# Optimization experiments

Measured on AMD Instinct MI355X. Metric: run time of the kernel, lower is better.

The kernel has to match this reference:

```python
import jax, jax.numpy as jnp
import numpy as np

N_NODES = 50000
N_EDGES = 500000


def setup_inputs() -> dict:
    key = jax.random.key(0)
    ks = jax.random.split(key, 24)
    p = {}
    p['x_feat'] = jax.random.normal(ks[0], (N_NODES, 24), dtype=jnp.float32)
    p['edge_index'] = jax.random.randint(ks[1], (2, N_EDGES), 0, N_NODES)
    p['edge_attr'] = jax.random.uniform(ks[2], (N_EDGES, 16), dtype=jnp.float32)
    def lin(k, fan_in, shape):
        b = 1.0 / np.sqrt(fan_in)
        return jax.random.uniform(k, shape, jnp.float32, -b, b)
    # group-0 input projection: 24 -> 32
    p['lin_prep_W'] = lin(ks[3], 24, (24, 32)); p['lin_prep_b'] = lin(ks[4], 24, (32,))
    # prep tube: 32 -> 16
    p['tube_W'] = lin(ks[5], 32, (32, 16)); p['tube_b'] = lin(ks[6], 32, (16,))
    # shared edge-attr trunk: 16 -> 32 -> 16
    p['edge_W1'] = lin(ks[7], 16, (16, 32)); p['edge_b1'] = lin(ks[8], 16, (32,))
    p['edge_W2'] = lin(ks[9], 32, (32, 16)); p['edge_b2'] = lin(ks[10], 32, (16,))
    # conv1: in=16, out=8 per aggr (mean, max, add)
    p['conv1_edge_W'] = lin(ks[11], 16, (3, 16, 16 * 8)); p['conv1_edge_b'] = lin(ks[12], 16, (3, 16 * 8))
    p['conv1_root_W'] = lin(ks[13], 16, (3, 16, 8)); p['conv1_bias'] = lin(ks[14], 16, (3, 8))
    # conv2: in=24, out=8 per aggr
    p['conv2_edge_W'] = lin(ks[15], 16, (3, 16, 24 * 8)); p['conv2_edge_b'] = lin(ks[16], 16, (3, 24 * 8))
    p['conv2_root_W'] = lin(ks[17], 24, (3, 24, 8)); p['conv2_bias'] = lin(ks[18], 24, (3, 8))
    # output head: 24 -> 2
    p['out_W'] = lin(ks[19], 24, (24, 2)); p['out_b'] = lin(ks[20], 24, (2,))
    return p


def _nnconv(x, e_repr, src, dst, edge_W, edge_b, root_W, bias, n_nodes):
    # x: [N, in]; e_repr: [E, 16]; edge_W: [3, 16, in*out]
    d_in = x.shape[1]
    x_src = x[src]  # [E, in]
    deg = jax.ops.segment_sum(jnp.ones_like(src, dtype=x.dtype), dst, num_segments=n_nodes)  # [N]
    outs = []
    for a, aggr in enumerate(('mean', 'max', 'add')):
        W_e = (e_repr @ edge_W[a] + edge_b[a]).reshape(e_repr.shape[0], d_in, -1)  # [E, in, out]
        msg = jnp.einsum('ei,eio->eo', x_src, W_e)  # [E, out]
        if aggr == 'add':
            agg = jax.ops.segment_sum(msg, dst, num_segments=n_nodes)
        elif aggr == 'mean':
            agg = jax.ops.segment_sum(msg, dst, num_segments=n_nodes) / jnp.maximum(deg, 1.0)[:, None]
        else:
            agg = jax.ops.segment_max(msg, dst, num_segments=n_nodes)
            agg = jnp.where(deg[:, None] > 0, agg, 0.0)  # no-neighbor nodes -> 0
        outs.append(agg + x @ root_W[a] + bias[a])
    return jax.nn.relu(jnp.concatenate(outs, axis=1))  # [N, 3*out]


def reference(x_feat, edge_index, edge_attr, lin_prep_W, lin_prep_b, tube_W, tube_b,
              edge_W1, edge_b1, edge_W2, edge_b2,
              conv1_edge_W, conv1_edge_b, conv1_root_W, conv1_bias,
              conv2_edge_W, conv2_edge_b, conv2_root_W, conv2_bias,
              out_W, out_b):
    n_nodes = x_feat.shape[0]
    src, dst = edge_index[0], edge_index[1]
    # node prep: group projection + tube (relu acts, dropout=0 -> identity)
    x = jax.nn.relu(x_feat @ lin_prep_W + lin_prep_b)       # [N, 32]
    x = jax.nn.relu(x @ tube_W + tube_b)                    # [N, 16]
    # shared edge-attr trunk (last activation = sigmoid), computed once
    e = jax.nn.relu(edge_attr @ edge_W1 + edge_b1)
    e_repr = jax.nn.sigmoid(e @ edge_W2 + edge_b2)          # [E, 16]
    # hop 1 and hop 2 of edge-conditioned NNConv with mean/max/add aggregators
    x = _nnconv(x, e_repr, src, dst, conv1_edge_W, conv1_edge_b, conv1_root_W, conv1_bias, n_nodes)  # [N, 24]
    x = _nnconv(x, e_repr, src, dst, conv2_edge_W, conv2_edge_b, conv2_root_W, conv2_bias, n_nodes)  # [N, 24]
    logits = x @ out_W + out_b                              # [N, 2]
    scores = jax.nn.softmax(logits, axis=1)
    return (logits, scores)
```

## Files before the change

### kernel.cpp

```cpp
#include <hip/hip_runtime.h>

#define BS 256

__device__ __forceinline__ unsigned short f2bf(float f) {
    unsigned x = __float_as_uint(f);
    return (unsigned short)((x + 0x7fffu + ((x >> 16) & 1u)) >> 16);
}
__device__ __forceinline__ unsigned pack2bf(float a, float b) {
    return (unsigned)f2bf(a) | ((unsigned)f2bf(b) << 16);
}
__device__ __forceinline__ void unpack2(unsigned u, float* d) {
    d[0] = __uint_as_float(u << 16);
    d[1] = __uint_as_float(u & 0xFFFF0000u);
}
__device__ __forceinline__ void unpack8(uint4 v, float* d) {
    unpack2(v.x, d); unpack2(v.y, d + 2); unpack2(v.z, d + 4); unpack2(v.w, d + 6);
}
__device__ __forceinline__ uint4 pack8bf(const float* r) {
    return make_uint4(pack2bf(r[0], r[1]), pack2bf(r[2], r[3]),
                      pack2bf(r[4], r[5]), pack2bf(r[6], r[7]));
}

__global__ __launch_bounds__(BS) void prep_deg_kernel(
    const float* __restrict__ xf,
    const float* __restrict__ W1, const float* __restrict__ b1,
    const float* __restrict__ W2, const float* __restrict__ b2,
    float* __restrict__ x16,
    const int* __restrict__ srcA, const int* __restrict__ dstA,
    int* __restrict__ cntS, int* __restrict__ cntD,
    int* __restrict__ jS, int* __restrict__ jD,
    int N, int E, int nbPrep)
{
    if ((int)blockIdx.x < nbPrep) {
        int n = blockIdx.x * BS + threadIdx.x;
        bool valid = n < N;
        int nn = valid ? n : 0;
        float a[24];
#pragma unroll
        for (int i = 0; i < 24; i += 4)
            *(float4*)(a + i) = *(const float4*)(xf + (size_t)nn * 24 + i);
        float h[32];
#pragma unroll
        for (int j = 0; j < 32; j++) {
            float s = b1[j];
#pragma unroll
            for (int i = 0; i < 24; i++) s = fmaf(a[i], W1[i * 32 + j], s);
            h[j] = fmaxf(s, 0.f);
        }
        if (!valid) return;
#pragma unroll
        for (int j = 0; j < 16; j++) {
            float s = b2[j];
#pragma unroll
            for (int i = 0; i < 32; i++) s = fmaf(h[i], W2[i * 16 + j], s);
            x16[(size_t)n * 16 + j] = fmaxf(s, 0.f);
        }
    } else {
        int tid = (blockIdx.x - nbPrep) * BS + threadIdx.x;
        if (tid < E) {
            jS[tid] = atomicAdd(&cntS[srcA[tid]], 1);
        } else if (tid < 2 * E) {
            int e = tid - E;
            jD[e] = atomicAdd(&cntD[dstA[e]], 1);
        }
    }
}

__global__ __launch_bounds__(BS) void offs_ynode16_kernel(
    const int* __restrict__ cntS, const int* __restrict__ cntD,
    int* __restrict__ offsS, int* __restrict__ offsD,
    int* __restrict__ cursS, int* __restrict__ cursD,
    const float* __restrict__ x,
    const float* __restrict__ W,
    const float* __restrict__ B,
    const float* __restrict__ RW,
    const float* __restrict__ RB,
    unsigned short* __restrict__ Y,
    float* __restrict__ root,
    int N, int nbOff, int nbY3)
{
    if ((int)blockIdx.x < nbOff) {
        int n = blockIdx.x * BS + threadIdx.x;
        int lane = threadIdx.x & 63;
        bool valid = n < N;
        int dS = valid ? cntS[n] : 0;
        int dD = valid ? cntD[n] : 0;
        int sS = dS, sD = dD;
#pragma unroll
        for (int o = 1; o < 64; o <<= 1) {
            int tS = __shfl_up(sS, o);
            int tD = __shfl_up(sD, o);
            if (lane >= o) { sS += tS; sD += tD; }
        }
        int totS = __shfl(sS, 63);
        int totD = __shfl(sD, 63);
        int baseS = 0, baseD = 0;
        if (lane == 63) {
            baseS = atomicAdd(cursS, totS);
            baseD = atomicAdd(cursD, totD);
        }
        baseS = __shfl(baseS, 63);
        baseD = __shfl(baseD, 63);
        if (valid) {
            offsS[n] = baseS + sS - dS;
            offsD[n] = baseD + sD - dD;
        }
    } else {
        const int IN = 16;
        __shared__ float w_lds[16 * 24];
        int t = threadIdx.x;
        int blk = blockIdx.x - nbOff;
        int kb = blk / nbY3;
        int xb = blk - kb * nbY3;

        for (int idx = t; idx < IN * 24; idx += BS) {
            int i = idx / 24;
            int j = idx - i * 24;
            int a = j >> 3, o = j & 7;
            float v;
            if (kb < 16)       v = W[(((size_t)a * 16 + kb) * IN + i) * 8 + o];
            else if (kb == 16) v = B[((size_t)a * IN + i) * 8 + o];
            else               v = RW[((size_t)a * IN + i) * 8 + o];
            w_lds[idx] = v;
        }
        __syncthreads();

        int tid = xb * BS + t;
        int n = tid / 3;
        int a = tid - n * 3;
        if (n >= N) return;

        float xv[IN];
#pragma unroll
        for (int i = 0; i < IN; i += 4)
            *(float4*)(xv + i) = *(const float4*)(x + (size_t)n * IN + i);

        float acc[8];
#pragma unroll
        for (int o = 0; o < 8; o++) acc[o] = 0.f;
        const float* wb = w_lds + a * 8;
#pragma unroll
        for (int i = 0; i < IN; i++) {
            float xi = xv[i];
#pragma unroll
            for (int o = 0; o < 8; o++)
                acc[o] = fmaf(xi, wb[i * 24 + o], acc[o]);
        }

        if (kb < 17) {
            *(uint4*)(Y + ((size_t)kb * N + n) * 24 + a * 8) = pack8bf(acc);
        } else {
            float* pr = root + (size_t)n * 24 + a * 8;
            *(float4*)(pr)     = make_float4(acc[0] + RB[a*8+0], acc[1] + RB[a*8+1],
                                             acc[2] + RB[a*8+2], acc[3] + RB[a*8+3]);
            *(float4*)(pr + 4) = make_float4(acc[4] + RB[a*8+4], acc[5] + RB[a*8+5],
                                             acc[6] + RB[a*8+6], acc[7] + RB[a*8+7]);
        }
    }
}

__global__ __launch_bounds__(BS) void er_fill_kernel(
    const int* __restrict__ srcA, const int* __restrict__ dstA,
    const int* __restrict__ jS, const int* __restrict__ jD,
    const int* __restrict__ offsS, const int* __restrict__ offsD,
    const float* __restrict__ eattr,
    const float* __restrict__ eW1, const float* __restrict__ eb1,
    const float* __restrict__ eW2, const float* __restrict__ eb2,
    uint4* __restrict__ erec, int E)
{
    int e = blockIdx.x * BS + threadIdx.x;
    if (e >= E) return;
    int s = srcA[e], d = dstA[e];
    int p = offsS[s] + jS[e];
    int q = offsD[d] + jD[e];

    float ea[16];
#pragma unroll
    for (int i = 0; i < 16; i += 4)
        *(float4*)(ea + i) = *(const float4*)(eattr + (size_t)e * 16 + i);
    float h[32];
#pragma unroll
    for (int j = 0; j < 32; j++) {
        float t = eb1[j];
#pragma unroll
        for (int i = 0; i < 16; i++) t = fmaf(ea[i], eW1[i * 32 + j], t);
        h[j] = fmaxf(t, 0.f);
    }
    float er[16];
#pragma unroll
    for (int j = 0; j < 16; j++) {
        float t = eb2[j];
#pragma unroll
        for (int i = 0; i < 32; i++) t = fmaf(h[i], eW2[i * 16 + j], t);
        er[j] = 1.f / (1.f + __expf(-t));
    }
    unsigned w[8];
#pragma unroll
    for (int j = 0; j < 8; j++) w[j] = pack2bf(er[2 * j], er[2 * j + 1]);
    uint4* rp = erec + (size_t)p * 4;
    rp[0] = make_uint4((unsigned)s, (unsigned)q, w[0], w[1]);
    rp[1] = make_uint4(w[2], w[3], w[4], w[5]);
    rp[2] = make_uint4(w[6], w[7], 0u, 0u);
    rp[3] = make_uint4(0u, 0u, 0u, 0u);
}

template <int IN>
__global__ __launch_bounds__(BS) void ynode_kernel(const float* __restrict__ x,
                                                   const float* __restrict__ W,
                                                   const float* __restrict__ B,
                                                   const float* __restrict__ RW,
                                                   const float* __restrict__ RB,
                                                   unsigned short* __restrict__ Y,
                                                   float* __restrict__ root, int N)
{
    __shared__ float w_lds[IN * 24];
    int t = threadIdx.x;
    int k = blockIdx.y;

    for (int idx = t; idx < IN * 24; idx += BS) {
        int i = idx / 24;
        int j = idx - i * 24;
        int a = j >> 3, o = j & 7;
        float v;
        if (k < 16)       v = W[(((size_t)a * 16 + k) * IN + i) * 8 + o];
        else if (k == 16) v = B[((size_t)a * IN + i) * 8 + o];
        else              v = RW[((size_t)a * IN + i) * 8 + o];
        w_lds[idx] = v;
    }
    __syncthreads();

    int tid = blockIdx.x * BS + t;
    int n = tid / 3;
    int a = tid - n * 3;
    if (n >= N) return;

    float xv[IN];
#pragma unroll
    for (int i = 0; i < IN; i += 4)
        *(float4*)(xv + i) = *(const float4*)(x + (size_t)n * IN + i);

    float acc[8];
#pragma unroll
    for (int o = 0; o < 8; o++) acc[o] = 0.f;
    const float* wb = w_lds + a * 8;
#pragma unroll
    for (int i = 0; i < IN; i++) {
        float xi = xv[i];
#pragma unroll
        for (int o = 0; o < 8; o++)
            acc[o] = fmaf(xi, wb[i * 24 + o], acc[o]);
    }

    if (k < 17) {
        *(uint4*)(Y + ((size_t)k * N + n) * 24 + a * 8) = pack8bf(acc);
    } else {
        float* pr = root + (size_t)n * 24 + a * 8;
        *(float4*)(pr)     = make_float4(acc[0] + RB[a*8+0], acc[1] + RB[a*8+1],
                                         acc[2] + RB[a*8+2], acc[3] + RB[a*8+3]);
        *(float4*)(pr + 4) = make_float4(acc[4] + RB[a*8+4], acc[5] + RB[a*8+5],
                                         acc[6] + RB[a*8+6], acc[7] + RB[a*8+7]);
    }
}

__global__ __launch_bounds__(BS) void msg_kernel(
    const uint4* __restrict__ erec,
    const unsigned short* __restrict__ Y,
    unsigned short* __restrict__ msg16,
    int N, int E)
{
    int tid = blockIdx.x * BS + threadIdx.x;
    int p = tid / 3;
    int j = tid - p * 3;
    if (p >= E) return;

    const uint4* rp = erec + (size_t)p * 4;
    uint4 r0 = rp[0];
    uint4 r1 = rp[1];
    uint4 r2 = rp[2];
    unsigned s = r0.x, q = r0.y;

    float er[16];
    unpack2(r0.z, er); unpack2(r0.w, er + 2);
    unpack8(r1, er + 4);
    unpack2(r2.x, er + 12); unpack2(r2.y, er + 14);

    const unsigned short* yb = Y + (size_t)s * 24 + j * 8;
    size_t kstride = (size_t)N * 24;

    float acc[8];
    unpack8(*(const uint4*)(yb + 16 * kstride), acc);
#pragma unroll
    for (int k = 0; k < 16; k++) {
        float t[8];
        unpack8(*(const uint4*)(yb + (size_t)k * kstride), t);
        float ek = er[k];
#pragma unroll
        for (int o = 0; o < 8; o++) acc[o] = fmaf(ek, t[o], acc[o]);
    }
    unsigned short* mrow = msg16 + (size_t)q * 32;
    *(uint4*)(mrow + j * 8) = pack8bf(acc);
    if (j == 0) *(uint4*)(mrow + 24) = make_uint4(0, 0, 0, 0);
}

template <bool FUSE_HEAD>
__global__ __launch_bounds__(BS) void gather_kernel(
    const unsigned short* __restrict__ msg16,
    const int* __restrict__ offs,
    const int* __restrict__ degi,
    const float* __restrict__ root,
    float* __restrict__ out,
    const float* __restrict__ oW, const float* __restrict__ ob,
    int N)
{
    int n = (blockIdx.x * BS + threadIdx.x) >> 6;
    if (n >= N) return;
    int lane = threadIdx.x & 63;
    int c = lane & 3;
    int r = lane >> 2;

    int off = offs[n];
    int d = degi[n];

    float s[8], m[8];
#pragma unroll
    for (int o = 0; o < 8; o++) { s[o] = 0.f; m[o] = -3.402823466e38f; }

    if (c < 3) {
        const unsigned short* base = msg16 + (size_t)off * 32 + c * 8;
        for (int j = r; j < d; j += 16) {
            uint4 v = *(const uint4*)(base + (size_t)j * 32);
            float t[8];
            unpack8(v, t);
#pragma unroll
            for (int o = 0; o < 8; o++) {
                s[o] += t[o];
                m[o] = fmaxf(m[o], t[o]);
            }
        }
    }
#pragma unroll
    for (int mask = 4; mask < 64; mask <<= 1) {
#pragma unroll
        for (int o = 0; o < 8; o++) {
            s[o] += __shfl_xor(s[o], mask);
            m[o] = fmaxf(m[o], __shfl_xor(m[o], mask));
        }
    }

    bool active = (lane < 3);
    float rr[8];
    if (active) {
        float inv = 1.f / fmaxf((float)d, 1.f);
        const float* pr = root + (size_t)n * 24 + lane * 8;
        float4 r0 = *(const float4*)(pr);
        float4 r1 = *(const float4*)(pr + 4);
        float rb[8] = {r0.x, r0.y, r0.z, r0.w, r1.x, r1.y, r1.z, r1.w};
#pragma unroll
        for (int o = 0; o < 8; o++) {
            float agg = (lane == 0) ? s[o] * inv
                      : (lane == 1) ? ((d > 0) ? m[o] : 0.f)
                      : s[o];
            rr[o] = fmaxf(rb[o] + agg, 0.f);
        }
    }

    if (!FUSE_HEAD) {
        if (active) {
            float* po = out + (size_t)n * 24 + lane * 8;
            *(float4*)(po)     = make_float4(rr[0], rr[1], rr[2], rr[3]);
            *(float4*)(po + 4) = make_float4(rr[4], rr[5], rr[6], rr[7]);
        }
    } else {
        float l0p = 0.f, l1p = 0.f;
        if (active) {
#pragma unroll
            for (int o = 0; o < 8; o++) {
                l0p = fmaf(rr[o], oW[(lane * 8 + o) * 2 + 0], l0p);
                l1p = fmaf(rr[o], oW[(lane * 8 + o) * 2 + 1], l1p);
            }
        }
        float l0 = __shfl(l0p, 0) + __shfl(l0p, 1) + __shfl(l0p, 2);
        float l1 = __shfl(l1p, 0) + __shfl(l1p, 1) + __shfl(l1p, 2);
        if (lane == 0) {
            l0 += ob[0]; l1 += ob[1];
            out[2 * (size_t)n + 0] = l0;
            out[2 * (size_t)n + 1] = l1;
            float mx = fmaxf(l0, l1);
            float e0 = __expf(l0 - mx), e1 = __expf(l1 - mx);
            float sm = e0 + e1;
            out[2 * (size_t)N + 2 * (size_t)n + 0] = e0 / sm;
            out[2 * (size_t)N + 2 * (size_t)n + 1] = e1 / sm;
        }
    }
}

extern "C" void kernel_launch(void* const* d_in, const int* in_sizes, int n_in,
                              void* d_out, int out_size, void* d_ws, size_t ws_size,
                              hipStream_t stream)
{
    const float* x_feat = (const float*)d_in[0];
    const int*   eidx   = (const int*)d_in[1];
    const float* eattr  = (const float*)d_in[2];
    const float* lpW = (const float*)d_in[3];
    const float* lpb = (const float*)d_in[4];
    const float* tW  = (const float*)d_in[5];
    const float* tb  = (const float*)d_in[6];
    const float* eW1 = (const float*)d_in[7];
    const float* eb1 = (const float*)d_in[8];
    const float* eW2 = (const float*)d_in[9];
    const float* eb2 = (const float*)d_in[10];
    const float* c1W = (const float*)d_in[11];
    const float* c1B = (const float*)d_in[12];
    const float* c1R = (const float*)d_in[13];
    const float* c1b = (const float*)d_in[14];
    const float* c2W = (const float*)d_in[15];
    const float* c2B = (const float*)d_in[16];
    const float* c2R = (const float*)d_in[17];
    const float* c2b = (const float*)d_in[18];
    const float* oW  = (const float*)d_in[19];
    const float* ob  = (const float*)d_in[20];

    int N = in_sizes[0] / 24;
    int E = in_sizes[1] / 2;
    const int* srcA = eidx;
    const int* dstA = eidx + E;

    char* wsb = (char*)d_ws;
    size_t off = 0;
    auto alloc = [&](size_t bytes) {
        off = (off + 255) & ~(size_t)255;
        void* p = wsb + off;
        off += bytes;
        return p;
    };
    unsigned short* Y     = (unsigned short*)alloc((size_t)17 * N * 24 * 2);
    unsigned short* msg16 = (unsigned short*)alloc((size_t)E * 32 * 2);
    uint4* erec = (uint4*)alloc((size_t)E * 64);
    float* root = (float*)alloc((size_t)N * 24 * 4);
    float* x16  = (float*)alloc((size_t)N * 16 * 4);
    float* x24a = (float*)alloc((size_t)N * 24 * 4);
    int* ibase  = (int*)alloc(((size_t)2 * N + 2) * 4);
    int* cntS = ibase;
    int* cntD = ibase + N;
    int* cursS = ibase + 2 * N;
    int* cursD = ibase + 2 * N + 1;
    int* offsS = (int*)alloc((size_t)N * 4);
    int* offsD = (int*)alloc((size_t)N * 4);
    int* jS    = (int*)alloc((size_t)E * 4);
    int* jD    = (int*)alloc((size_t)E * 4);

    dim3 blk(BS);
    int nb_nodes = (N + BS - 1) / BS;
    int nb_deg2  = (2 * E + BS - 1) / BS;
    int nb_edges = (E + BS - 1) / BS;
    int nb_msg   = (3 * E + BS - 1) / BS;
    int nb_gath  = ((size_t)N * 64 + BS - 1) / BS;
    int nb_y3    = (3 * N + BS - 1) / BS;
    int nbY      = nb_y3 * 18;
    dim3 ygrid(nb_y3, 18);

    hipMemsetAsync(ibase, 0, (2 * (size_t)N + 2) * 4, stream);

    prep_deg_kernel<<<nb_nodes + nb_deg2, blk, 0, stream>>>(
        x_feat, lpW, lpb, tW, tb, x16, srcA, dstA, cntS, cntD, jS, jD, N, E, nb_nodes);

    offs_ynode16_kernel<<<nb_nodes + nbY, blk, 0, stream>>>(
        cntS, cntD, offsS, offsD, cursS, cursD,
        x16, c1W, c1B, c1R, c1b, Y, root, N, nb_nodes, nb_y3);

    er_fill_kernel<<<nb_edges, blk, 0, stream>>>(srcA, dstA, jS, jD, offsS, offsD,
                                                 eattr, eW1, eb1, eW2, eb2, erec, E);

    msg_kernel<<<nb_msg, blk, 0, stream>>>(erec, Y, msg16, N, E);
    gather_kernel<false><<<nb_gath, blk, 0, stream>>>(msg16, offsD, cntD, root, x24a,
                                                      oW, ob, N);

    ynode_kernel<24><<<ygrid, blk, 0, stream>>>(x24a, c2W, c2B, c2R, c2b, Y, root, N);
    msg_kernel<<<nb_msg, blk, 0, stream>>>(erec, Y, msg16, N, E);
    gather_kernel<true><<<nb_gath, blk, 0, stream>>>(msg16, offsD, cntD, root,
                                                     (float*)d_out, oW, ob, N);
}
```

Before: 264.7 us.

## Move edge MLP into degree-count kernel to overlap with atomics

The per-edge MLP (16->32->16 with sigmoid) moves out of the fill kernel and into the first kernel, running as extra blocks alongside the degree atomics and the node prep. Its result goes to a new bf16 buffer, and the fill kernel now only reads those packed values and scatters them into the CSR records. The aim is to hide the edge MLP's compute behind the latency-bound atomic counting. The cost is an extra 32 bytes per edge of global write and read traffic.

```diff
diff --git a/kernel.cpp b/kernel.cpp
--- a/kernel.cpp
+++ b/kernel.cpp
@@ -21,7 +21,7 @@
                       pack2bf(r[4], r[5]), pack2bf(r[6], r[7]));
 }
 
-__global__ __launch_bounds__(BS) void prep_deg_kernel(
+__global__ __launch_bounds__(BS) void prep_deg_er_kernel(
     const float* __restrict__ xf,
     const float* __restrict__ W1, const float* __restrict__ b1,
     const float* __restrict__ W2, const float* __restrict__ b2,
@@ -29,39 +29,70 @@
     const int* __restrict__ srcA, const int* __restrict__ dstA,
     int* __restrict__ cntS, int* __restrict__ cntD,
     int* __restrict__ jS, int* __restrict__ jD,
-    int N, int E, int nbPrep)
-{
-    if ((int)blockIdx.x < nbPrep) {
-        int n = blockIdx.x * BS + threadIdx.x;
-        bool valid = n < N;
-        int nn = valid ? n : 0;
-        float a[24];
-#pragma unroll
-        for (int i = 0; i < 24; i += 4)
-            *(float4*)(a + i) = *(const float4*)(xf + (size_t)nn * 24 + i);
-        float h[32];
-#pragma unroll
-        for (int j = 0; j < 32; j++) {
-            float s = b1[j];
-#pragma unroll
-            for (int i = 0; i < 24; i++) s = fmaf(a[i], W1[i * 32 + j], s);
-            h[j] = fmaxf(s, 0.f);
-        }
-        if (!valid) return;
-#pragma unroll
-        for (int j = 0; j < 16; j++) {
-            float s = b2[j];
-#pragma unroll
-            for (int i = 0; i < 32; i++) s = fmaf(h[i], W2[i * 16 + j], s);
-            x16[(size_t)n * 16 + j] = fmaxf(s, 0.f);
-        }
-    } else {
-        int tid = (blockIdx.x - nbPrep) * BS + threadIdx.x;
+    const float* __restrict__ eattr,
+    const float* __restrict__ eW1, const float* __restrict__ eb1,
+    const float* __restrict__ eW2, const float* __restrict__ eb2,
+    unsigned short* __restrict__ er_e,
+    int N, int E, int nbDeg2, int nbEdges)
+{
+    int bx = blockIdx.x;
+    if (bx < nbDeg2) {
+        int tid = bx * BS + threadIdx.x;
         if (tid < E) {
             jS[tid] = atomicAdd(&cntS[srcA[tid]], 1);
         } else if (tid < 2 * E) {
             int e = tid - E;
             jD[e] = atomicAdd(&cntD[dstA[e]], 1);
+        }
+    } else if (bx < nbDeg2 + nbEdges) {
+        int e = (bx - nbDeg2) * BS + threadIdx.x;
+        if (e >= E) return;
+        float ea[16];
+#pragma unroll
+        for (int i = 0; i < 16; i += 4)
+            *(float4*)(ea + i) = *(const float4*)(eattr + (size_t)e * 16 + i);
+        float h[32];
+#pragma unroll
+        for (int j = 0; j < 32; j++) {
+            float t = eb1[j];
+#pragma unroll
+            for (int i = 0; i < 16; i++) t = fmaf(ea[i], eW1[i * 32 + j], t);
+            h[j] = fmaxf(t, 0.f);
+        }
+        float er[16];
+#pragma unroll
+        for (int j = 0; j < 16; j++) {
+            float t = eb2[j];
+#pragma unroll
+            for (int i = 0; i < 32; i++) t = fmaf(h[i], eW2[i * 16 + j], t);
+            er[j] = 1.f / (1.f + __expf(-t));
+        }
+        uint4* qo = (uint4*)(er_e + (size_t)e * 16);
+        qo[0] = pack8bf(er);
+        qo[1] = pack8bf(er + 8);
+    } else {
+        int n = (bx - nbDeg2 - nbEdges) * BS + threadIdx.x;
+        bool valid = n < N;
+        int nn = valid ? n : 0;
+        float a[24];
+#pragma unroll
+        for (int i = 0; i < 24; i += 4)
+            *(float4*)(a + i) = *(const float4*)(xf + (size_t)nn * 24 + i);
+        float h[32];
+#pragma unroll
+        for (int j = 0; j < 32; j++) {
+            float s = b1[j];
+#pragma unroll
+            for (int i = 0; i < 24; i++) s = fmaf(a[i], W1[i * 32 + j], s);
+            h[j] = fmaxf(s, 0.f);
+        }
+        if (!valid) return;
+#pragma unroll
+        for (int j = 0; j < 16; j++) {
+            float s = b2[j];
+#pragma unroll
+            for (int i = 0; i < 32; i++) s = fmaf(h[i], W2[i * 16 + j], s);
+            x16[(size_t)n * 16 + j] = fmaxf(s, 0.f);
         }
     }
 }
@@ -159,13 +190,11 @@
     }
 }
 
-__global__ __launch_bounds__(BS) void er_fill_kernel(
+__global__ __launch_bounds__(BS) void fill_kernel(
     const int* __restrict__ srcA, const int* __restrict__ dstA,
     const int* __restrict__ jS, const int* __restrict__ jD,
     const int* __restrict__ offsS, const int* __restrict__ offsD,
-    const float* __restrict__ eattr,
-    const float* __restrict__ eW1, const float* __restrict__ eb1,
-    const float* __restrict__ eW2, const float* __restrict__ eb2,
+    const unsigned short* __restrict__ er_e,
     uint4* __restrict__ erec, int E)
 {
     int e = blockIdx.x * BS + threadIdx.x;
@@ -173,34 +202,13 @@
     int s = srcA[e], d = dstA[e];
     int p = offsS[s] + jS[e];
     int q = offsD[d] + jD[e];
-
-    float ea[16];
-#pragma unroll
-    for (int i = 0; i < 16; i += 4)
-        *(float4*)(ea + i) = *(const float4*)(eattr + (size_t)e * 16 + i);
-    float h[32];
-#pragma unroll
-    for (int j = 0; j < 32; j++) {
-        float t = eb1[j];
-#pragma unroll
-        for (int i = 0; i < 16; i++) t = fmaf(ea[i], eW1[i * 32 + j], t);
-        h[j] = fmaxf(t, 0.f);
-    }
-    float er[16];
-#pragma unroll
-    for (int j = 0; j < 16; j++) {
-        float t = eb2[j];
-#pragma unroll
-        for (int i = 0; i < 32; i++) t = fmaf(h[i], eW2[i * 16 + j], t);
-        er[j] = 1.f / (1.f + __expf(-t));
-    }
-    unsigned w[8];
-#pragma unroll
-    for (int j = 0; j < 8; j++) w[j] = pack2bf(er[2 * j], er[2 * j + 1]);
+    const uint4* ei = (const uint4*)(er_e + (size_t)e * 16);
+    uint4 e0 = ei[0];
+    uint4 e1 = ei[1];
     uint4* rp = erec + (size_t)p * 4;
-    rp[0] = make_uint4((unsigned)s, (unsigned)q, w[0], w[1]);
-    rp[1] = make_uint4(w[2], w[3], w[4], w[5]);
-    rp[2] = make_uint4(w[6], w[7], 0u, 0u);
+    rp[0] = make_uint4((unsigned)s, (unsigned)q, e0.x, e0.y);
+    rp[1] = make_uint4(e0.z, e0.w, e1.x, e1.y);
+    rp[2] = make_uint4(e1.z, e1.w, 0u, 0u);
     rp[3] = make_uint4(0u, 0u, 0u, 0u);
 }
 
@@ -436,6 +444,7 @@
     unsigned short* Y     = (unsigned short*)alloc((size_t)17 * N * 24 * 2);
     unsigned short* msg16 = (unsigned short*)alloc((size_t)E * 32 * 2);
     uint4* erec = (uint4*)alloc((size_t)E * 64);
+    unsigned short* er_e  = (unsigned short*)alloc((size_t)E * 16 * 2);
     float* root = (float*)alloc((size_t)N * 24 * 4);
     float* x16  = (float*)alloc((size_t)N * 16 * 4);
     float* x24a = (float*)alloc((size_t)N * 24 * 4);
@@ -461,15 +470,16 @@
 
     hipMemsetAsync(ibase, 0, (2 * (size_t)N + 2) * 4, stream);
 
-    prep_deg_kernel<<<nb_nodes + nb_deg2, blk, 0, stream>>>(
-        x_feat, lpW, lpb, tW, tb, x16, srcA, dstA, cntS, cntD, jS, jD, N, E, nb_nodes);
+    prep_deg_er_kernel<<<nb_deg2 + nb_edges + nb_nodes, blk, 0, stream>>>(
+        x_feat, lpW, lpb, tW, tb, x16, srcA, dstA, cntS, cntD, jS, jD,
+        eattr, eW1, eb1, eW2, eb2, er_e, N, E, nb_deg2, nb_edges);
 
     offs_ynode16_kernel<<<nb_nodes + nbY, blk, 0, stream>>>(
         cntS, cntD, offsS, offsD, cursS, cursD,
         x16, c1W, c1B, c1R, c1b, Y, root, N, nb_nodes, nb_y3);
 
-    er_fill_kernel<<<nb_edges, blk, 0, stream>>>(srcA, dstA, jS, jD, offsS, offsD,
-                                                 eattr, eW1, eb1, eW2, eb2, erec, E);
+    fill_kernel<<<nb_edges, blk, 0, stream>>>(srcA, dstA, jS, jD, offsS, offsD,
+                                              er_e, erec, E);
 
     msg_kernel<<<nb_msg, blk, 0, stream>>>(erec, Y, msg16, N, E);
     gather_kernel<false><<<nb_gath, blk, 0, stream>>>(msg16, offsD, cntD, root, x24a,
```

Measured after the change: 278.9 us. 1.05x slower.
